# Kernel optimization log

Hardware: AMD Instinct MI355X
Metric: run time of the kernel (lower is better)

Reference implementation:

```python
import jax, jax.numpy as jnp
import numpy as np

B, N, V, H, R, A, IN, K = 64, 512, 64, 512, 4, 18, 128, 32
EPS = 1e-8


def setup_inputs() -> dict:
    key = jax.random.key(0)
    ks = jax.random.split(key, 20)
    g = lambda i, shape, s=1.0: jax.random.normal(ks[i], shape, jnp.float32) * s
    u = lambda i, shape: jax.random.uniform(ks[i], shape, dtype=jnp.float32)
    cin = IN + R * V
    return dict(
        x=g(0, (B, IN)),
        h=g(1, (B, H), 0.1),
        c=g(2, (B, H), 0.1),
        memory=g(3, (B, N, V), 0.1),
        read_weights=u(4, (B, R, N)),
        write_weights=u(5, (B, N)),
        usage=u(6, (B, N)),
        link_matrix=u(7, (B, N, N)) * 0.01,
        precedence_weights=u(8, (B, N)),
        W_ih=g(9, (4 * H, cin), 0.05), W_hh=g(10, (4 * H, H), 0.05),
        b_ih=jnp.zeros(4 * H, jnp.float32), b_hh=jnp.zeros(4 * H, jnp.float32),
        W_read=g(11, (R, V + 4, H), 0.05), b_read=jnp.zeros((R, V + 4), jnp.float32),
        W_write=g(12, (3 * V + 3, H), 0.05), b_write=jnp.zeros(3 * V + 3, jnp.float32),
        W_pol=g(13, (A, H), 0.05), b_pol=jnp.zeros(A, jnp.float32),
        W_val=g(14, (1, H), 0.05), b_val=jnp.zeros(1, jnp.float32),
    )


def reference(x, h, c, memory, read_weights, write_weights, usage, link_matrix,
              precedence_weights, W_ih, W_hh, b_ih, b_hh, W_read, b_read,
              W_write, b_write, W_pol, b_pol, W_val, b_val):
    # ---- read heads (vectorized over R) ----
    ro = jnp.einsum('roh,bh->bro', W_read, h) + b_read            # [B,R,V+4]
    rkey = ro[..., :V]
    rbeta = jax.nn.softplus(ro[..., V])                           # [B,R]
    rpi = jax.nn.softmax(ro[..., V + 1:V + 4], axis=-1)           # backward/content/forward gates
    mem_norm = jnp.maximum(jnp.linalg.norm(memory, axis=-1), EPS)  # [B,N]
    key_norm = jnp.maximum(jnp.linalg.norm(rkey, axis=-1), EPS)    # [B,R]
    sim = jnp.einsum('bnv,brv->brn', memory, rkey) / (mem_norm[:, None, :] * key_norm[..., None])
    scores = rbeta[..., None] * sim                                # [B,R,N]
    kth = jax.lax.top_k(scores, K)[0][..., -1:]                    # sparse top-k mask
    cw = jax.nn.softmax(jnp.where(scores >= kth, scores, -jnp.inf), axis=-1)
    fw = jnp.einsum('bnm,brm->brn', link_matrix, read_weights)     # forward weighting L w
    bw = jnp.einsum('bmn,brm->brn', link_matrix, read_weights)     # backward weighting L^T w
    w_r = rpi[..., 0:1] * bw + rpi[..., 1:2] * cw + rpi[..., 2:3] * fw  # [B,R,N]
    rvec = jnp.einsum('brn,bnv->brv', w_r, memory).reshape(B, R * V)
    # ---- LSTM controller (torch LSTMCell gate order i,f,g,o) ----
    gates = jnp.concatenate([x, rvec], -1) @ W_ih.T + h @ W_hh.T + b_ih + b_hh
    i_g, f_g, g_g, o_g = jnp.split(gates, 4, axis=-1)
    c_new = jax.nn.sigmoid(f_g) * c + jax.nn.sigmoid(i_g) * jnp.tanh(g_g)
    h_new = jax.nn.sigmoid(o_g) * jnp.tanh(c_new)
    # ---- write head ----
    wo = h_new @ W_write.T + b_write                               # [B,3V+3]
    wkey = wo[:, :V]
    erase = jax.nn.sigmoid(wo[:, V:2 * V])
    add = jnp.tanh(wo[:, 2 * V:3 * V])
    wbeta = jax.nn.softplus(wo[:, 3 * V])
    g_a = jax.nn.sigmoid(wo[:, 3 * V + 1])
    g_w = jax.nn.sigmoid(wo[:, 3 * V + 2])
    wkey_norm = jnp.maximum(jnp.linalg.norm(wkey, axis=-1), EPS)
    wsim = jnp.einsum('bnv,bv->bn', memory, wkey) / (mem_norm * wkey_norm[:, None])
    cw_w = jax.nn.softmax(wbeta[:, None] * wsim, axis=-1)
    # allocation weighting from sorted usage (DNC Eq. 1)
    idx = jnp.argsort(usage, axis=-1)
    u_sorted = jnp.take_along_axis(usage, idx, -1)
    prod_prev = jnp.concatenate([jnp.ones((B, 1), usage.dtype), jnp.cumprod(u_sorted, -1)[:, :-1]], -1)
    a_sorted = (1.0 - u_sorted) * prod_prev
    alloc = jnp.take_along_axis(a_sorted, jnp.argsort(idx, -1), -1)
    write_w = g_w[:, None] * (g_a[:, None] * alloc + (1.0 - g_a)[:, None] * cw_w)  # [B,N]
    # ---- memory erase/add ----
    mem_new = memory * (1.0 - write_w[:, :, None] * erase[:, None, :]) + write_w[:, :, None] * add[:, None, :]
    # ---- usage (psi detached as in torch.no_grad) ----
    psi = jax.lax.stop_gradient(jnp.prod(1.0 - w_r, axis=1))
    usage_new = (usage + write_weights - usage * write_weights) * psi
    # ---- link matrix + precedence ----
    ws = jnp.sum(write_w, -1, keepdims=True)
    prec_new = (1.0 - ws) * precedence_weights + write_w
    decay = (1.0 - write_w[:, :, None]) * (1.0 - write_w[:, None, :])
    link_new = decay * link_matrix + write_w[:, :, None] * precedence_weights[:, None, :]
    link_new = link_new * (1.0 - jnp.eye(N, dtype=link_new.dtype))
    # ---- actor/critic heads ----
    logits = h_new @ W_pol.T + b_pol
    value = h_new @ W_val.T + b_val
    return (logits, value, h_new, c_new, mem_new, w_r, write_w, usage_new, link_new, prec_new)
```

## Files before the change

kernel.cpp:

```cpp
#include <hip/hip_runtime.h>
#include <math.h>

constexpr int Bb = 64, Nn = 512, Vv = 64, Hh = 512, Rr = 4, Aa = 18, INp = 128, KTOP = 32;
constexpr int CIN = 384;
constexpr int WOUT = 195;
#define EPSf 1e-8f

__device__ __forceinline__ float sigmoidf(float x){ return 1.f/(1.f+expf(-x)); }
__device__ __forceinline__ float softplusf(float x){ return (x>20.f)? x : log1pf(expf(x)); }
__device__ __forceinline__ float wave_reduce(float v){
  #pragma unroll
  for(int o=32;o>0;o>>=1) v += __shfl_down(v, o, 64);
  return v;
}
__device__ __forceinline__ unsigned f2ord(float f){
  unsigned u = __float_as_uint(f);
  return (u & 0x80000000u) ? ~u : (u | 0x80000000u);
}

__global__ void k_stage1(const float* __restrict__ link, const float* __restrict__ rw,
                         const float* __restrict__ Wr, const float* __restrict__ brd,
                         const float* __restrict__ h, const float* __restrict__ mem,
                         float* __restrict__ fw, float* __restrict__ bwpart,
                         float* __restrict__ rvec, float* __restrict__ rp,
                         float* __restrict__ cw) {
  __shared__ __align__(16) float smem[8192];
  if (blockIdx.x < 512) {
    float (*bl)[4][512] = reinterpret_cast<float (*)[4][512]>(smem);
    if (blockIdx.x < 64) rvec[blockIdx.x*256 + threadIdx.x] = 0.f;
    int b  = blockIdx.x >> 3;
    int ch = blockIdx.x & 7;
    int wv = threadIdx.x >> 6, lane = threadIdx.x & 63;
    const float* rwb = rw + b*Rr*Nn;
    float rwv[4][8];
    #pragma unroll
    for (int r = 0; r < 4; ++r)
      #pragma unroll
      for (int t = 0; t < 8; ++t) rwv[r][t] = rwb[r*512 + lane + 64*t];
    float bwacc[8][4] = {};
    const float* lb = link + (size_t)b*Nn*Nn;
    int n0 = ch*64 + wv*16;
    for (int i = 0; i < 16; ++i) {
      int n = n0 + i;
      float lk[8];
      #pragma unroll
      for (int t = 0; t < 8; ++t) lk[t] = lb[n*512 + lane + 64*t];
      float s0 = rwb[n], s1 = rwb[512+n], s2 = rwb[1024+n], s3 = rwb[1536+n];
      float f0=0,f1=0,f2=0,f3=0;
      #pragma unroll
      for (int t = 0; t < 8; ++t) {
        float lv = lk[t];
        f0 += lv*rwv[0][t]; f1 += lv*rwv[1][t]; f2 += lv*rwv[2][t]; f3 += lv*rwv[3][t];
        bwacc[t][0] += lv*s0; bwacc[t][1] += lv*s1; bwacc[t][2] += lv*s2; bwacc[t][3] += lv*s3;
      }
      f0 = wave_reduce(f0); f1 = wave_reduce(f1);
      f2 = wave_reduce(f2); f3 = wave_reduce(f3);
      if (lane == 0) {
        fw[(b*Rr+0)*Nn+n] = f0; fw[(b*Rr+1)*Nn+n] = f1;
        fw[(b*Rr+2)*Nn+n] = f2; fw[(b*Rr+3)*Nn+n] = f3;
      }
    }
    #pragma unroll
    for (int t = 0; t < 8; ++t)
      #pragma unroll
      for (int r = 0; r < 4; ++r) bl[wv][r][lane + 64*t] = bwacc[t][r];
    __syncthreads();
    int tid = threadIdx.x;
    #pragma unroll
    for (int q = 0; q < 8; ++q) {
      int idx = q*256 + tid;
      int r = idx >> 9, j = idx & 511;
      float v = bl[0][r][j] + bl[1][r][j] + bl[2][r][j] + bl[3][r][j];
      bwpart[((size_t)(ch*Bb + b)*Rr + r)*Nn + j] = v;
    }
  } else {
    float* sh  = smem;
    float* sro = smem + 512;
    unsigned long long* sk = (unsigned long long*)(smem + 592);
    float* sred = smem + 1616;
    float* skv  = smem + 1620;
    int blk = blockIdx.x - 512;
    int b = blk >> 2, r = blk & 3;
    int tid = threadIdx.x;
    int wv = tid >> 6, lane = tid & 63;
    const float* hb = h + b*Hh;
    for (int i = tid; i < 512; i += 256) sh[i] = hb[i];
    __syncthreads();
    const float* wbase = Wr + (size_t)(r*68)*Hh;
    int pbase = wv*17;
    #pragma unroll
    for (int g = 0; g < 4; ++g) {
      int p = pbase + g*4;
      const float *w0 = wbase + (size_t)p*Hh, *w1 = w0 + Hh, *w2 = w1 + Hh, *w3 = w2 + Hh;
      float a0=0,a1=0,a2=0,a3=0;
      #pragma unroll
      for (int t = 0; t < 8; ++t) {
        int k = lane + 64*t; float hv = sh[k];
        a0 += w0[k]*hv; a1 += w1[k]*hv; a2 += w2[k]*hv; a3 += w3[k]*hv;
      }
      #pragma unroll
      for (int o = 32; o > 0; o >>= 1) {
        a0 += __shfl_down(a0,o,64); a1 += __shfl_down(a1,o,64);
        a2 += __shfl_down(a2,o,64); a3 += __shfl_down(a3,o,64);
      }
      if (lane == 0) {
        sro[p]   = a0 + brd[r*68+p];   sro[p+1] = a1 + brd[r*68+p+1];
        sro[p+2] = a2 + brd[r*68+p+2]; sro[p+3] = a3 + brd[r*68+p+3];
      }
    }
    {
      int p = pbase + 16;
      const float* w0 = wbase + (size_t)p*Hh;
      float a0 = 0.f;
      #pragma unroll
      for (int t = 0; t < 8; ++t) { int k = lane + 64*t; a0 += w0[k]*sh[k]; }
      a0 = wave_reduce(a0);
      if (lane == 0) sro[p] = a0 + brd[r*68+p];
    }
    __syncthreads();
    if (wv == 0) {
      float kv = sro[lane];
      float k2 = wave_reduce(kv*kv);
      if (lane == 0) {
        float rbeta = softplusf(sro[64]);
        float sc = rbeta / fmaxf(sqrtf(k2), EPSf);
        float e0 = sro[65], e1 = sro[66], e2 = sro[67];
        float mm = fmaxf(e0, fmaxf(e1, e2));
        float x0 = expf(e0-mm), x1 = expf(e1-mm), x2 = expf(e2-mm);
        float inv = 1.f/(x0+x1+x2);
        float* rpb = rp + (b*4 + r)*4;
        rpb[0] = sc; rpb[1] = x0*inv; rpb[2] = x1*inv; rpb[3] = x2*inv;
        sro[68] = sc;
      }
    }
    __syncthreads();
    float sc = sro[68];
    const float4* key4 = (const float4*)sro;
    float v0, v1;
    {
      const float4* m4 = (const float4*)(mem + ((size_t)(b*Nn + tid))*Vv);
      float dot=0.f, nrm=0.f;
      #pragma unroll
      for (int i = 0; i < 16; ++i) {
        float4 mv = m4[i]; float4 kk = key4[i];
        dot += mv.x*kk.x + mv.y*kk.y + mv.z*kk.z + mv.w*kk.w;
        nrm += mv.x*mv.x + mv.y*mv.y + mv.z*mv.z + mv.w*mv.w;
      }
      v0 = sc * dot / fmaxf(sqrtf(nrm), EPSf);
    }
    {
      const float4* m4 = (const float4*)(mem + ((size_t)(b*Nn + tid + 256))*Vv);
      float dot=0.f, nrm=0.f;
      #pragma unroll
      for (int i = 0; i < 16; ++i) {
        float4 mv = m4[i]; float4 kk = key4[i];
        dot += mv.x*kk.x + mv.y*kk.y + mv.z*kk.z + mv.w*kk.w;
        nrm += mv.x*mv.x + mv.y*mv.y + mv.z*mv.z + mv.w*mv.w;
      }
      v1 = sc * dot / fmaxf(sqrtf(nrm), EPSf);
    }
    unsigned long long k0 = ((unsigned long long)f2ord(v0) << 32) | (unsigned)(511 - tid);
    unsigned long long k1 = ((unsigned long long)f2ord(v1) << 32) | (unsigned)(255 - tid);
    sk[tid] = k0; sk[tid+256] = k1;
    __syncthreads();
    int c0 = 0, c1 = 0;
    #pragma unroll 8
    for (int j = 0; j < 512; ++j) {
      unsigned long long kj = sk[j];
      c0 += (kj > k0); c1 += (kj > k1);
    }
    if (c0 == KTOP-1) skv[0] = v0;
    if (c1 == KTOP-1) skv[0] = v1;
    if (c0 == 0) skv[1] = v0;
    if (c1 == 0) skv[1] = v1;
    __syncthreads();
    float kth = skv[0], mx = skv[1];
    float e0 = (v0 >= kth) ? expf(v0-mx) : 0.f;
    float e1 = (v1 >= kth) ? expf(v1-mx) : 0.f;
    float s = wave_reduce(e0+e1);
    if (lane == 0) sred[wv] = s;
    __syncthreads();
    float inv = 1.f/(sred[0]+sred[1]+sred[2]+sred[3]);
    int brr = b*4 + r;
    cw[brr*Nn+tid]     = e0*inv;
    cw[brr*Nn+tid+256] = e1*inv;
  }
}

__global__ void k_wrrv(const float* __restrict__ bwpart, const float* __restrict__ cw,
                       const float* __restrict__ fw, const float* __restrict__ rp,
                       const float* __restrict__ usage, const float* __restrict__ wwt,
                       const float* __restrict__ mem,
                       float* __restrict__ out_wr, float* __restrict__ out_usage,
                       float* __restrict__ rvec) {
  __shared__ float swr[4][256];
  int b = blockIdx.x >> 1, ch = blockIdx.x & 1;
  int tid = threadIdx.x;
  int n = ch*256 + tid;
  int idx = b*Nn + n;
  float psi = 1.f;
  #pragma unroll
  for (int r = 0; r < 4; ++r) {
    int brr = b*4 + r;
    float bwv = 0.f;
    #pragma unroll
    for (int chh = 0; chh < 8; ++chh)
      bwv += bwpart[((size_t)(chh*Bb + b)*Rr + r)*Nn + n];
    const float* rpb = rp + brr*4;
    float w = rpb[1]*bwv + rpb[2]*cw[brr*Nn+n] + rpb[3]*fw[brr*Nn+n];
    out_wr[brr*Nn+n] = w;
    swr[r][tid] = w;
    psi *= (1.f - w);
  }
  float u = usage[idx], wt = wwt[idx];
  out_usage[idx] = (u + wt - u*wt) * psi;
  __syncthreads();
  int r = tid >> 6, v = tid & 63;
  const float* mb = mem + ((size_t)b*Nn + ch*256)*Vv + v;
  float acc = 0.f;
  #pragma unroll 16
  for (int t = 0; t < 256; ++t) acc += swr[r][t] * mb[t*Vv];
  atomicAdd(&rvec[(b*4+r)*Vv + v], acc);
}

__global__ void k_gates_lstm(const float* __restrict__ x, const float* __restrict__ rvec,
                             const float* __restrict__ h, const float* __restrict__ Wih,
                             const float* __restrict__ Whh, const float* __restrict__ bih,
                             const float* __restrict__ bhh, const float* __restrict__ c,
                             float* __restrict__ out_h, float* __restrict__ out_c) {
  int gid = blockIdx.x*4 + (threadIdx.x>>6);
  int lane = threadIdx.x & 63;
  int hh = gid >> 4;
  int bt = gid & 15;
  float acc[4][4] = {};
  #pragma unroll
  for (int t = 0; t < 6; ++t) {
    int k = lane + 64*t;
    float u[4], w[4];
    #pragma unroll
    for (int i = 0; i < 4; ++i) {
      int b = bt*4 + i;
      u[i] = (k < INp) ? x[b*INp + k] : rvec[b*(Rr*Vv) + k - INp];
      w[i] = Wih[(size_t)(i*Hh + hh)*CIN + k];
    }
    #pragma unroll
    for (int g = 0; g < 4; ++g)
      #pragma unroll
      for (int bb = 0; bb < 4; ++bb) acc[g][bb] += w[g]*u[bb];
  }
  #pragma unroll
  for (int t = 0; t < 8; ++t) {
    int k = lane + 64*t;
    float u[4], w[4];
    #pragma unroll
    for (int i = 0; i < 4; ++i) {
      u[i] = h[(bt*4+i)*Hh + k];
      w[i] = Whh[(size_t)(i*Hh + hh)*Hh + k];
    }
    #pragma unroll
    for (int g = 0; g < 4; ++g)
      #pragma unroll
      for (int bb = 0; bb < 4; ++bb) acc[g][bb] += w[g]*u[bb];
  }
  #pragma unroll
  for (int g = 0; g < 4; ++g)
    #pragma unroll
    for (int bb = 0; bb < 4; ++bb) acc[g][bb] = wave_reduce(acc[g][bb]);
  if (lane == 0) {
    float bsum[4];
    #pragma unroll
    for (int g = 0; g < 4; ++g) bsum[g] = bih[g*Hh + hh] + bhh[g*Hh + hh];
    #pragma unroll
    for (int bb = 0; bb < 4; ++bb) {
      int b = bt*4 + bb;
      float ig = sigmoidf(acc[0][bb] + bsum[0]);
      float fg = sigmoidf(acc[1][bb] + bsum[1]);
      float gg = tanhf   (acc[2][bb] + bsum[2]);
      float og = sigmoidf(acc[3][bb] + bsum[3]);
      float cn = fg * c[b*Hh + hh] + ig * gg;
      float hn = og * tanhf(cn);
      out_c[b*Hh + hh] = cn;
      out_h[b*Hh + hh] = hn;
    }
  }
}

__global__ void k_tail(const float* __restrict__ hn, const float* __restrict__ Ww,
                       const float* __restrict__ bw_, const float* __restrict__ Wp,
                       const float* __restrict__ bp, const float* __restrict__ Wv,
                       const float* __restrict__ bv, const float* __restrict__ usage,
                       const float* __restrict__ prec, const float* __restrict__ mem,
                       float* __restrict__ wo, float* __restrict__ out_logits,
                       float* __restrict__ out_value, float* __restrict__ out_ww,
                       float* __restrict__ out_prec) {
  __shared__ __align__(16) float sh[512];
  __shared__ __align__(16) float swo[200];
  __shared__ unsigned long long sk[512];
  __shared__ float su[512];
  __shared__ float cp[512];
  __shared__ float sred[8];
  int b = blockIdx.x, tid = threadIdx.x;
  int wv = tid >> 6, lane = tid & 63;
  const float* hb = hn + b*Hh;
  for (int i = tid; i < 512; i += 256) sh[i] = hb[i];
  __syncthreads();
  int dbeg = wv*54, dend = (dbeg + 54 < 214) ? dbeg + 54 : 214;
  for (int p = dbeg; p < dend; p += 4) {
    int d1 = (p+1 < 213) ? p+1 : 213, d2 = (p+2 < 213) ? p+2 : 213, d3 = (p+3 < 213) ? p+3 : 213;
    const float* w0 = (p  < WOUT) ? Ww + (size_t)p *Hh : ((p  < WOUT+Aa) ? Wp + (size_t)(p -WOUT)*Hh : Wv);
    const float* w1 = (d1 < WOUT) ? Ww + (size_t)d1*Hh : ((d1 < WOUT+Aa) ? Wp + (size_t)(d1-WOUT)*Hh : Wv);
    const float* w2 = (d2 < WOUT) ? Ww + (size_t)d2*Hh : ((d2 < WOUT+Aa) ? Wp + (size_t)(d2-WOUT)*Hh : Wv);
    const float* w3 = (d3 < WOUT) ? Ww + (size_t)d3*Hh : ((d3 < WOUT+Aa) ? Wp + (size_t)(d3-WOUT)*Hh : Wv);
    float a0=0,a1=0,a2=0,a3=0;
    #pragma unroll
    for (int t = 0; t < 8; ++t) {
      int k = lane + 64*t; float hv = sh[k];
      a0 += w0[k]*hv; a1 += w1[k]*hv; a2 += w2[k]*hv; a3 += w3[k]*hv;
    }
    #pragma unroll
    for (int o = 32; o > 0; o >>= 1) {
      a0 += __shfl_down(a0,o,64); a1 += __shfl_down(a1,o,64);
      a2 += __shfl_down(a2,o,64); a3 += __shfl_down(a3,o,64);
    }
    if (lane == 0) {
      float av[4] = {a0,a1,a2,a3};
      #pragma unroll
      for (int i = 0; i < 4; ++i) {
        int d = p + i;
        if (d >= dend) break;
        float a = av[i];
        if (d < WOUT)          { float vv = a + bw_[d]; swo[d] = vv; wo[b*WOUT+d] = vv; }
        else if (d < WOUT+Aa)  { out_logits[b*Aa + (d-WOUT)] = a + bp[d-WOUT]; }
        else                   { out_value[b] = a + bv[0]; }
      }
    }
  }
  __syncthreads();
  float wbeta = softplusf(swo[192]);
  const float4* key4 = (const float4*)swo;
  float s0, s1;
  {
    const float4* m4 = (const float4*)(mem + ((size_t)(b*Nn + tid))*Vv);
    float dot=0.f, nrm=0.f, kn=0.f;
    #pragma unroll
    for (int i = 0; i < 16; ++i) {
      float4 mv = m4[i]; float4 kk = key4[i];
      dot += mv.x*kk.x + mv.y*kk.y + mv.z*kk.z + mv.w*kk.w;
      nrm += mv.x*mv.x + mv.y*mv.y + mv.z*mv.z + mv.w*mv.w;
      kn  += kk.x*kk.x + kk.y*kk.y + kk.z*kk.z + kk.w*kk.w;
    }
    s0 = wbeta * dot / (fmaxf(sqrtf(nrm), EPSf) * fmaxf(sqrtf(kn), EPSf));
  }
  {
    const float4* m4 = (const float4*)(mem + ((size_t)(b*Nn + tid + 256))*Vv);
    float dot=0.f, nrm=0.f, kn=0.f;
    #pragma unroll
    for (int i = 0; i < 16; ++i) {
      float4 mv = m4[i]; float4 kk = key4[i];
      dot += mv.x*kk.x + mv.y*kk.y + mv.z*kk.z + mv.w*kk.w;
      nrm += mv.x*mv.x + mv.y*mv.y + mv.z*mv.z + mv.w*mv.w;
      kn  += kk.x*kk.x + kk.y*kk.y + kk.z*kk.z + kk.w*kk.w;
    }
    s1 = wbeta * dot / (fmaxf(sqrtf(nrm), EPSf) * fmaxf(sqrtf(kn), EPSf));
  }
  float u0 = usage[b*Nn+tid], u1 = usage[b*Nn+tid+256];
  unsigned long long k0 = ((unsigned long long)f2ord(u0) << 32) | (unsigned)tid;
  unsigned long long k1 = ((unsigned long long)f2ord(u1) << 32) | (unsigned)(tid+256);
  sk[tid] = k0; sk[tid+256] = k1;
  float mxl = fmaxf(s0, s1);
  #pragma unroll
  for (int o = 32; o > 0; o >>= 1) mxl = fmaxf(mxl, __shfl_down(mxl,o,64));
  if (lane == 0) sred[wv] = mxl;
  __syncthreads();
  float mx = fmaxf(fmaxf(sred[0],sred[1]), fmaxf(sred[2],sred[3]));
  float e0 = expf(s0-mx), e1 = expf(s1-mx);
  float ssum = wave_reduce(e0+e1);
  if (lane == 0) sred[4+wv] = ssum;
  int r0 = 0, r1 = 0;
  #pragma unroll 8
  for (int j = 0; j < 512; ++j) {
    unsigned long long kj = sk[j];
    r0 += (kj < k0); r1 += (kj < k1);
  }
  __syncthreads();
  float cinv = 1.f/(sred[4]+sred[5]+sred[6]+sred[7]);
  float c0 = e0*cinv, c1 = e1*cinv;
  su[r0] = u0; su[r1] = u1;
  __syncthreads();
  cp[tid] = su[tid]; cp[tid+256] = su[tid+256];
  __syncthreads();
  for (int d = 1; d < 512; d <<= 1) {
    float t0 = cp[tid]     * ((tid >= d)     ? cp[tid-d]     : 1.f);
    float t1 = cp[tid+256] * ((tid+256 >= d) ? cp[tid+256-d] : 1.f);
    __syncthreads();
    cp[tid] = t0; cp[tid+256] = t1;
    __syncthreads();
  }
  float pp0 = (r0 == 0) ? 1.f : cp[r0-1];
  float pp1 = (r1 == 0) ? 1.f : cp[r1-1];
  float a0 = (1.f-u0)*pp0, a1 = (1.f-u1)*pp1;
  float ga = sigmoidf(swo[193]);
  float gw = sigmoidf(swo[194]);
  float wv0 = gw * (ga*a0 + (1.f-ga)*c0);
  float wv1 = gw * (ga*a1 + (1.f-ga)*c1);
  out_ww[b*Nn+tid]     = wv0;
  out_ww[b*Nn+tid+256] = wv1;
  float ws_ = wave_reduce(wv0+wv1);
  if (lane == 0) sred[wv] = ws_;
  __syncthreads();
  float wsum = sred[0]+sred[1]+sred[2]+sred[3];
  out_prec[b*Nn+tid]     = (1.f-wsum)*prec[b*Nn+tid]     + wv0;
  out_prec[b*Nn+tid+256] = (1.f-wsum)*prec[b*Nn+tid+256] + wv1;
}

__global__ void k_memlink(const float* __restrict__ link, const float* __restrict__ ww,
                          const float* __restrict__ prec, const float* __restrict__ mem,
                          const float* __restrict__ wo, float* __restrict__ out_link,
                          float* __restrict__ out_mem) {
  int bid = blockIdx.x;
  if (bid < 16384) {
    int idx4 = bid*256 + threadIdx.x;
    int base = idx4*4;
    int b = base >> 18;
    int rem = base & 262143;
    int i = rem >> 9;
    int j0 = rem & 511;
    float wi = ww[b*Nn + i];
    float fi = 1.f - wi;
    float4 lv = *(const float4*)(link + base);
    float4 wj = *(const float4*)(ww + b*Nn + j0);
    float4 pj = *(const float4*)(prec + b*Nn + j0);
    float4 o;
    o.x = fi*(1.f-wj.x)*lv.x + wi*pj.x;
    o.y = fi*(1.f-wj.y)*lv.y + wi*pj.y;
    o.z = fi*(1.f-wj.z)*lv.z + wi*pj.z;
    o.w = fi*(1.f-wj.w)*lv.w + wi*pj.w;
    if (i >= j0 && i < j0+4) {
      if (i == j0) o.x = 0.f;
      else if (i == j0+1) o.y = 0.f;
      else if (i == j0+2) o.z = 0.f;
      else o.w = 0.f;
    }
    *(float4*)(out_link + base) = o;
  } else {
    int idx4 = (bid - 16384)*256 + threadIdx.x;
    int base = idx4*4;
    int b = base >> 15;
    int rem = base & 32767;
    int n = rem >> 6;
    int v0 = rem & 63;
    float w = ww[b*Nn + n];
    const float* wob = wo + b*WOUT;
    float4 m = *(const float4*)(mem + base);
    float4 o;
    float e, a;
    e = sigmoidf(wob[64+v0+0]); a = tanhf(wob[128+v0+0]); o.x = m.x*(1.f-w*e)+w*a;
    e = sigmoidf(wob[64+v0+1]); a = tanhf(wob[128+v0+1]); o.y = m.y*(1.f-w*e)+w*a;
    e = sigmoidf(wob[64+v0+2]); a = tanhf(wob[128+v0+2]); o.z = m.z*(1.f-w*e)+w*a;
    e = sigmoidf(wob[64+v0+3]); a = tanhf(wob[128+v0+3]); o.w = m.w*(1.f-w*e)+w*a;
    *(float4*)(out_mem + base) = o;
  }
}

extern "C" void kernel_launch(void* const* d_in, const int* in_sizes, int n_in,
                              void* d_out, int out_size, void* d_ws, size_t ws_size,
                              hipStream_t stream) {
  const float* x    = (const float*)d_in[0];
  const float* h    = (const float*)d_in[1];
  const float* c    = (const float*)d_in[2];
  const float* mem  = (const float*)d_in[3];
  const float* rw   = (const float*)d_in[4];
  const float* wwt  = (const float*)d_in[5];
  const float* usage= (const float*)d_in[6];
  const float* link = (const float*)d_in[7];
  const float* prec = (const float*)d_in[8];
  const float* Wih  = (const float*)d_in[9];
  const float* Whh  = (const float*)d_in[10];
  const float* bih  = (const float*)d_in[11];
  const float* bhh  = (const float*)d_in[12];
  const float* Wr   = (const float*)d_in[13];
  const float* br   = (const float*)d_in[14];
  const float* Ww   = (const float*)d_in[15];
  const float* bw_  = (const float*)d_in[16];
  const float* Wp   = (const float*)d_in[17];
  const float* bp   = (const float*)d_in[18];
  const float* Wv   = (const float*)d_in[19];
  const float* bv   = (const float*)d_in[20];

  float* out = (float*)d_out;
  float* o_logits = out + 0;
  float* o_value  = out + 1152;
  float* o_h      = out + 1216;
  float* o_c      = out + 33984;
  float* o_mem    = out + 66752;
  float* o_wr     = out + 2163904;
  float* o_ww     = out + 2294976;
  float* o_usage  = out + 2327744;
  float* o_link   = out + 2360512;
  float* o_prec   = out + 19137728;

  float* ws = (float*)d_ws;
  float* ws_rp     = ws;
  float* ws_cw     = ws + 1024;
  float* ws_fw     = ws + 132096;
  float* ws_bwpart = ws + 263168;
  float* ws_rvec   = ws + 1311744;
  float* ws_wo     = ws + 1328128;

  k_stage1     <<<dim3(768),        dim3(256), 0, stream>>>(link, rw, Wr, br, h, mem, ws_fw, ws_bwpart, ws_rvec, ws_rp, ws_cw);
  k_wrrv       <<<dim3(Bb*2),       dim3(256), 0, stream>>>(ws_bwpart, ws_cw, ws_fw, ws_rp, usage, wwt, mem, o_wr, o_usage, ws_rvec);
  k_gates_lstm <<<dim3(2048),       dim3(256), 0, stream>>>(x, ws_rvec, h, Wih, Whh, bih, bhh, c, o_h, o_c);
  k_tail       <<<dim3(Bb),         dim3(256), 0, stream>>>(o_h, Ww, bw_, Wp, bp, Wv, bv, usage, prec, mem, ws_wo, o_logits, o_value, o_ww, o_prec);
  k_memlink    <<<dim3(16384+2048), dim3(256), 0, stream>>>(link, o_ww, prec, mem, ws_wo, o_link, o_mem);
}
```

Measured before the change: 285.4 us.

## Increase parallelism in link read, read-vector and tail kernels with float4 loads

The link-matrix pass in stage1 is split into 16 chunks per batch instead of 8 and switches to float4 loads. The backward-weight partial buffer doubles, and the workspace offsets for rvec and wo move to make room. k_wrrv now uses 8 blocks per batch with one thread per (head, row), which raises occupancy. k_tail runs 512 threads so each thread handles one memory row, halving serial work in the rank sort and scan at the cost of more per-block threads and extra partial-sum reads.

```diff
diff --git a/kernel.cpp b/kernel.cpp
--- a/kernel.cpp
+++ b/kernel.cpp
@@ -25,53 +25,76 @@
                          float* __restrict__ rvec, float* __restrict__ rp,
                          float* __restrict__ cw) {
   __shared__ __align__(16) float smem[8192];
-  if (blockIdx.x < 512) {
-    float (*bl)[4][512] = reinterpret_cast<float (*)[4][512]>(smem);
+  if (blockIdx.x < 1024) {
+    float4 (*bl4)[4][128] = reinterpret_cast<float4 (*)[4][128]>(smem);
     if (blockIdx.x < 64) rvec[blockIdx.x*256 + threadIdx.x] = 0.f;
-    int b  = blockIdx.x >> 3;
-    int ch = blockIdx.x & 7;
+    int b  = blockIdx.x >> 4;
+    int ch = blockIdx.x & 15;
     int wv = threadIdx.x >> 6, lane = threadIdx.x & 63;
     const float* rwb = rw + b*Rr*Nn;
-    float rwv[4][8];
-    #pragma unroll
-    for (int r = 0; r < 4; ++r)
-      #pragma unroll
-      for (int t = 0; t < 8; ++t) rwv[r][t] = rwb[r*512 + lane + 64*t];
-    float bwacc[8][4] = {};
-    const float* lb = link + (size_t)b*Nn*Nn;
-    int n0 = ch*64 + wv*16;
-    for (int i = 0; i < 16; ++i) {
+    const float4* rw4 = (const float4*)rwb;
+    float4 rwv4[4][2];
+    #pragma unroll
+    for (int r = 0; r < 4; ++r) {
+      rwv4[r][0] = rw4[r*128 + lane];
+      rwv4[r][1] = rw4[r*128 + 64 + lane];
+    }
+    float4 bwacc[2][4];
+    #pragma unroll
+    for (int t = 0; t < 2; ++t)
+      #pragma unroll
+      for (int r = 0; r < 4; ++r) bwacc[t][r] = make_float4(0.f,0.f,0.f,0.f);
+    const float4* lb4 = (const float4*)(link + (size_t)b*Nn*Nn);
+    int n0 = ch*32 + wv*8;
+    #pragma unroll 2
+    for (int i = 0; i < 8; ++i) {
       int n = n0 + i;
-      float lk[8];
-      #pragma unroll
-      for (int t = 0; t < 8; ++t) lk[t] = lb[n*512 + lane + 64*t];
+      float4 A = lb4[n*128 + lane];
+      float4 Bv = lb4[n*128 + 64 + lane];
       float s0 = rwb[n], s1 = rwb[512+n], s2 = rwb[1024+n], s3 = rwb[1536+n];
-      float f0=0,f1=0,f2=0,f3=0;
-      #pragma unroll
-      for (int t = 0; t < 8; ++t) {
-        float lv = lk[t];
-        f0 += lv*rwv[0][t]; f1 += lv*rwv[1][t]; f2 += lv*rwv[2][t]; f3 += lv*rwv[3][t];
-        bwacc[t][0] += lv*s0; bwacc[t][1] += lv*s1; bwacc[t][2] += lv*s2; bwacc[t][3] += lv*s3;
-      }
-      f0 = wave_reduce(f0); f1 = wave_reduce(f1);
-      f2 = wave_reduce(f2); f3 = wave_reduce(f3);
+      float f0 = A.x*rwv4[0][0].x + A.y*rwv4[0][0].y + A.z*rwv4[0][0].z + A.w*rwv4[0][0].w
+               + Bv.x*rwv4[0][1].x + Bv.y*rwv4[0][1].y + Bv.z*rwv4[0][1].z + Bv.w*rwv4[0][1].w;
+      float f1 = A.x*rwv4[1][0].x + A.y*rwv4[1][0].y + A.z*rwv4[1][0].z + A.w*rwv4[1][0].w
+               + Bv.x*rwv4[1][1].x + Bv.y*rwv4[1][1].y + Bv.z*rwv4[1][1].z + Bv.w*rwv4[1][1].w;
+      float f2 = A.x*rwv4[2][0].x + A.y*rwv4[2][0].y + A.z*rwv4[2][0].z + A.w*rwv4[2][0].w
+               + Bv.x*rwv4[2][1].x + Bv.y*rwv4[2][1].y + Bv.z*rwv4[2][1].z + Bv.w*rwv4[2][1].w;
+      float f3 = A.x*rwv4[3][0].x + A.y*rwv4[3][0].y + A.z*rwv4[3][0].z + A.w*rwv4[3][0].w
+               + Bv.x*rwv4[3][1].x + Bv.y*rwv4[3][1].y + Bv.z*rwv4[3][1].z + Bv.w*rwv4[3][1].w;
+      bwacc[0][0].x += A.x*s0; bwacc[0][0].y += A.y*s0; bwacc[0][0].z += A.z*s0; bwacc[0][0].w += A.w*s0;
+      bwacc[0][1].x += A.x*s1; bwacc[0][1].y += A.y*s1; bwacc[0][1].z += A.z*s1; bwacc[0][1].w += A.w*s1;
+      bwacc[0][2].x += A.x*s2; bwacc[0][2].y += A.y*s2; bwacc[0][2].z += A.z*s2; bwacc[0][2].w += A.w*s2;
+      bwacc[0][3].x += A.x*s3; bwacc[0][3].y += A.y*s3; bwacc[0][3].z += A.z*s3; bwacc[0][3].w += A.w*s3;
+      bwacc[1][0].x += Bv.x*s0; bwacc[1][0].y += Bv.y*s0; bwacc[1][0].z += Bv.z*s0; bwacc[1][0].w += Bv.w*s0;
+      bwacc[1][1].x += Bv.x*s1; bwacc[1][1].y += Bv.y*s1; bwacc[1][1].z += Bv.z*s1; bwacc[1][1].w += Bv.w*s1;
+      bwacc[1][2].x += Bv.x*s2; bwacc[1][2].y += Bv.y*s2; bwacc[1][2].z += Bv.z*s2; bwacc[1][2].w += Bv.w*s2;
+      bwacc[1][3].x += Bv.x*s3; bwacc[1][3].y += Bv.y*s3; bwacc[1][3].z += Bv.z*s3; bwacc[1][3].w += Bv.w*s3;
+      #pragma unroll
+      for (int o = 32; o > 0; o >>= 1) {
+        f0 += __shfl_down(f0,o,64); f1 += __shfl_down(f1,o,64);
+        f2 += __shfl_down(f2,o,64); f3 += __shfl_down(f3,o,64);
+      }
       if (lane == 0) {
         fw[(b*Rr+0)*Nn+n] = f0; fw[(b*Rr+1)*Nn+n] = f1;
         fw[(b*Rr+2)*Nn+n] = f2; fw[(b*Rr+3)*Nn+n] = f3;
       }
     }
     #pragma unroll
-    for (int t = 0; t < 8; ++t)
-      #pragma unroll
-      for (int r = 0; r < 4; ++r) bl[wv][r][lane + 64*t] = bwacc[t][r];
+    for (int r = 0; r < 4; ++r) {
+      bl4[wv][r][lane]      = bwacc[0][r];
+      bl4[wv][r][64 + lane] = bwacc[1][r];
+    }
     __syncthreads();
     int tid = threadIdx.x;
-    #pragma unroll
-    for (int q = 0; q < 8; ++q) {
-      int idx = q*256 + tid;
-      int r = idx >> 9, j = idx & 511;
-      float v = bl[0][r][j] + bl[1][r][j] + bl[2][r][j] + bl[3][r][j];
-      bwpart[((size_t)(ch*Bb + b)*Rr + r)*Nn + j] = v;
+    float4* bwp4 = (float4*)bwpart;
+    #pragma unroll
+    for (int q = 0; q < 2; ++q) {
+      int fid = q*256 + tid;
+      int r = fid >> 7, j4 = fid & 127;
+      float4 a = bl4[0][r][j4], bb = bl4[1][r][j4], cc = bl4[2][r][j4], dd = bl4[3][r][j4];
+      float4 v;
+      v.x = a.x+bb.x+cc.x+dd.x; v.y = a.y+bb.y+cc.y+dd.y;
+      v.z = a.z+bb.z+cc.z+dd.z; v.w = a.w+bb.w+cc.w+dd.w;
+      bwp4[((size_t)(ch*Bb + b)*Rr + r)*128 + j4] = v;
     }
   } else {
     float* sh  = smem;
@@ -79,7 +102,7 @@
     unsigned long long* sk = (unsigned long long*)(smem + 592);
     float* sred = smem + 1616;
     float* skv  = smem + 1620;
-    int blk = blockIdx.x - 512;
+    int blk = blockIdx.x - 1024;
     int b = blk >> 2, r = blk & 3;
     int tid = threadIdx.x;
     int wv = tid >> 6, lane = tid & 63;
@@ -193,34 +216,32 @@
                        const float* __restrict__ mem,
                        float* __restrict__ out_wr, float* __restrict__ out_usage,
                        float* __restrict__ rvec) {
-  __shared__ float swr[4][256];
-  int b = blockIdx.x >> 1, ch = blockIdx.x & 1;
+  __shared__ float swr[4][64];
+  int b = blockIdx.x >> 3, ch = blockIdx.x & 7;
   int tid = threadIdx.x;
-  int n = ch*256 + tid;
-  int idx = b*Nn + n;
-  float psi = 1.f;
-  #pragma unroll
-  for (int r = 0; r < 4; ++r) {
-    int brr = b*4 + r;
-    float bwv = 0.f;
-    #pragma unroll
-    for (int chh = 0; chh < 8; ++chh)
-      bwv += bwpart[((size_t)(chh*Bb + b)*Rr + r)*Nn + n];
-    const float* rpb = rp + brr*4;
-    float w = rpb[1]*bwv + rpb[2]*cw[brr*Nn+n] + rpb[3]*fw[brr*Nn+n];
-    out_wr[brr*Nn+n] = w;
-    swr[r][tid] = w;
-    psi *= (1.f - w);
-  }
-  float u = usage[idx], wt = wwt[idx];
-  out_usage[idx] = (u + wt - u*wt) * psi;
-  __syncthreads();
-  int r = tid >> 6, v = tid & 63;
-  const float* mb = mem + ((size_t)b*Nn + ch*256)*Vv + v;
+  int r = tid >> 6, nl = tid & 63;
+  int n = ch*64 + nl;
+  int brr = b*4 + r;
+  float bwv = 0.f;
+  #pragma unroll
+  for (int chh = 0; chh < 16; ++chh)
+    bwv += bwpart[((size_t)(chh*Bb + b)*Rr + r)*Nn + n];
+  const float* rpb = rp + brr*4;
+  float w = rpb[1]*bwv + rpb[2]*cw[brr*Nn+n] + rpb[3]*fw[brr*Nn+n];
+  out_wr[brr*Nn+n] = w;
+  swr[r][nl] = w;
+  __syncthreads();
+  if (tid < 64) {
+    int idx = b*Nn + ch*64 + tid;
+    float psi = (1.f-swr[0][tid])*(1.f-swr[1][tid])*(1.f-swr[2][tid])*(1.f-swr[3][tid]);
+    float u = usage[idx], wt = wwt[idx];
+    out_usage[idx] = (u + wt - u*wt) * psi;
+  }
+  const float* mb = mem + ((size_t)b*Nn + ch*64)*Vv + nl;
   float acc = 0.f;
   #pragma unroll 16
-  for (int t = 0; t < 256; ++t) acc += swr[r][t] * mb[t*Vv];
-  atomicAdd(&rvec[(b*4+r)*Vv + v], acc);
+  for (int t = 0; t < 64; ++t) acc += swr[r][t] * mb[t*Vv];
+  atomicAdd(&rvec[brr*Vv + nl], acc);
 }
 
 __global__ void k_gates_lstm(const float* __restrict__ x, const float* __restrict__ rvec,
@@ -298,13 +319,13 @@
   __shared__ unsigned long long sk[512];
   __shared__ float su[512];
   __shared__ float cp[512];
-  __shared__ float sred[8];
+  __shared__ float sred[16];
   int b = blockIdx.x, tid = threadIdx.x;
   int wv = tid >> 6, lane = tid & 63;
   const float* hb = hn + b*Hh;
-  for (int i = tid; i < 512; i += 256) sh[i] = hb[i];
-  __syncthreads();
-  int dbeg = wv*54, dend = (dbeg + 54 < 214) ? dbeg + 54 : 214;
+  if (tid < 512) sh[tid] = hb[tid];
+  __syncthreads();
+  int dbeg = wv*27, dend = (dbeg + 27 < 214) ? dbeg + 27 : 214;
   for (int p = dbeg; p < dend; p += 4) {
     int d1 = (p+1 < 213) ? p+1 : 213, d2 = (p+2 < 213) ? p+2 : 213, d3 = (p+3 < 213) ? p+3 : 213;
     const float* w0 = (p  < WOUT) ? Ww + (size_t)p *Hh : ((p  < WOUT+Aa) ? Wp + (size_t)(p -WOUT)*Hh : Wv);
@@ -338,7 +359,7 @@
   __syncthreads();
   float wbeta = softplusf(swo[192]);
   const float4* key4 = (const float4*)swo;
-  float s0, s1;
+  float s0;
   {
     const float4* m4 = (const float4*)(mem + ((size_t)(b*Nn + tid))*Vv);
     float dot=0.f, nrm=0.f, kn=0.f;
@@ -351,66 +372,54 @@
     }
     s0 = wbeta * dot / (fmaxf(sqrtf(nrm), EPSf) * fmaxf(sqrtf(kn), EPSf));
   }
-  {
-    const float4* m4 = (const float4*)(mem + ((size_t)(b*Nn + tid + 256))*Vv);
-    float dot=0.f, nrm=0.f, kn=0.f;
-    #pragma unroll
-    for (int i = 0; i < 16; ++i) {
-      float4 mv = m4[i]; float4 kk = key4[i];
-      dot += mv.x*kk.x + mv.y*kk.y + mv.z*kk.z + mv.w*kk.w;
-      nrm += mv.x*mv.x + mv.y*mv.y + mv.z*mv.z + mv.w*mv.w;
-      kn  += kk.x*kk.x + kk.y*kk.y + kk.z*kk.z + kk.w*kk.w;
-    }
-    s1 = wbeta * dot / (fmaxf(sqrtf(nrm), EPSf) * fmaxf(sqrtf(kn), EPSf));
-  }
-  float u0 = usage[b*Nn+tid], u1 = usage[b*Nn+tid+256];
+  float u0 = usage[b*Nn+tid];
   unsigned long long k0 = ((unsigned long long)f2ord(u0) << 32) | (unsigned)tid;
-  unsigned long long k1 = ((unsigned long long)f2ord(u1) << 32) | (unsigned)(tid+256);
-  sk[tid] = k0; sk[tid+256] = k1;
-  float mxl = fmaxf(s0, s1);
+  sk[tid] = k0;
+  float mxl = s0;
   #pragma unroll
   for (int o = 32; o > 0; o >>= 1) mxl = fmaxf(mxl, __shfl_down(mxl,o,64));
   if (lane == 0) sred[wv] = mxl;
   __syncthreads();
-  float mx = fmaxf(fmaxf(sred[0],sred[1]), fmaxf(sred[2],sred[3]));
-  float e0 = expf(s0-mx), e1 = expf(s1-mx);
-  float ssum = wave_reduce(e0+e1);
-  if (lane == 0) sred[4+wv] = ssum;
-  int r0 = 0, r1 = 0;
+  float mx = sred[0];
+  #pragma unroll
+  for (int i = 1; i < 8; ++i) mx = fmaxf(mx, sred[i]);
+  float e0 = expf(s0-mx);
+  float ssum = wave_reduce(e0);
+  if (lane == 0) sred[8+wv] = ssum;
+  int r0 = 0;
   #pragma unroll 8
   for (int j = 0; j < 512; ++j) {
     unsigned long long kj = sk[j];
-    r0 += (kj < k0); r1 += (kj < k1);
-  }
-  __syncthreads();
-  float cinv = 1.f/(sred[4]+sred[5]+sred[6]+sred[7]);
-  float c0 = e0*cinv, c1 = e1*cinv;
-  su[r0] = u0; su[r1] = u1;
-  __syncthreads();
-  cp[tid] = su[tid]; cp[tid+256] = su[tid+256];
+    r0 += (kj < k0);
+  }
+  __syncthreads();
+  float tot = 0.f;
+  #pragma unroll
+  for (int i = 0; i < 8; ++i) tot += sred[8+i];
+  float c0 = e0 / tot;
+  su[r0] = u0;
+  __syncthreads();
+  cp[tid] = su[tid];
   __syncthreads();
   for (int d = 1; d < 512; d <<= 1) {
-    float t0 = cp[tid]     * ((tid >= d)     ? cp[tid-d]     : 1.f);
-    float t1 = cp[tid+256] * ((tid+256 >= d) ? cp[tid+256-d] : 1.f);
-    __syncthreads();
-    cp[tid] = t0; cp[tid+256] = t1;
+    float t0 = cp[tid] * ((tid >= d) ? cp[tid-d] : 1.f);
+    __syncthreads();
+    cp[tid] = t0;
     __syncthreads();
   }
   float pp0 = (r0 == 0) ? 1.f : cp[r0-1];
-  float pp1 = (r1 == 0) ? 1.f : cp[r1-1];
-  float a0 = (1.f-u0)*pp0, a1 = (1.f-u1)*pp1;
+  float a0 = (1.f-u0)*pp0;
   float ga = sigmoidf(swo[193]);
   float gw = sigmoidf(swo[194]);
   float wv0 = gw * (ga*a0 + (1.f-ga)*c0);
-  float wv1 = gw * (ga*a1 + (1.f-ga)*c1);
-  out_ww[b*Nn+tid]     = wv0;
-  out_ww[b*Nn+tid+256] = wv1;
-  float ws_ = wave_reduce(wv0+wv1);
+  out_ww[b*Nn+tid] = wv0;
+  float ws_ = wave_reduce(wv0);
   if (lane == 0) sred[wv] = ws_;
   __syncthreads();
-  float wsum = sred[0]+sred[1]+sred[2]+sred[3];
-  out_prec[b*Nn+tid]     = (1.f-wsum)*prec[b*Nn+tid]     + wv0;
-  out_prec[b*Nn+tid+256] = (1.f-wsum)*prec[b*Nn+tid+256] + wv1;
+  float wsum = 0.f;
+  #pragma unroll
+  for (int i = 0; i < 8; ++i) wsum += sred[i];
+  out_prec[b*Nn+tid] = (1.f-wsum)*prec[b*Nn+tid] + wv0;
 }
 
 __global__ void k_memlink(const float* __restrict__ link, const float* __restrict__ ww,
@@ -504,12 +513,12 @@
   float* ws_cw     = ws + 1024;
   float* ws_fw     = ws + 132096;
   float* ws_bwpart = ws + 263168;
-  float* ws_rvec   = ws + 1311744;
-  float* ws_wo     = ws + 1328128;
-
-  k_stage1     <<<dim3(768),        dim3(256), 0, stream>>>(link, rw, Wr, br, h, mem, ws_fw, ws_bwpart, ws_rvec, ws_rp, ws_cw);
-  k_wrrv       <<<dim3(Bb*2),       dim3(256), 0, stream>>>(ws_bwpart, ws_cw, ws_fw, ws_rp, usage, wwt, mem, o_wr, o_usage, ws_rvec);
+  float* ws_rvec   = ws + 2360320;
+  float* ws_wo     = ws + 2376704;
+
+  k_stage1     <<<dim3(1280),       dim3(256), 0, stream>>>(link, rw, Wr, br, h, mem, ws_fw, ws_bwpart, ws_rvec, ws_rp, ws_cw);
+  k_wrrv       <<<dim3(Bb*8),       dim3(256), 0, stream>>>(ws_bwpart, ws_cw, ws_fw, ws_rp, usage, wwt, mem, o_wr, o_usage, ws_rvec);
   k_gates_lstm <<<dim3(2048),       dim3(256), 0, stream>>>(x, ws_rvec, h, Wih, Whh, bih, bhh, c, o_h, o_c);
-  k_tail       <<<dim3(Bb),         dim3(256), 0, stream>>>(o_h, Ww, bw_, Wp, bp, Wv, bv, usage, prec, mem, ws_wo, o_logits, o_value, o_ww, o_prec);
+  k_tail       <<<dim3(Bb),         dim3(512), 0, stream>>>(o_h, Ww, bw_, Wp, bp, Wv, bv, usage, prec, mem, ws_wo, o_logits, o_value, o_ww, o_prec);
   k_memlink    <<<dim3(16384+2048), dim3(256), 0, stream>>>(link, o_ww, prec, mem, ws_wo, o_link, o_mem);
 }
```

Result: slower. 355.6 us (+24.6%).
